# Kernel tuning notes

Hardware: AMD Instinct MI355X
Metric: run time of the kernel (lower is better)

The kernel has to match this reference:

```python
import jax, jax.numpy as jnp
import numpy as np

D_MODEL = 1024
NUM_HEADS = 16
HEAD_DIM = D_MODEL // NUM_HEADS
SCALE = HEAD_DIM ** -0.5
LN_EPS = 1e-5
Q_EPS = 1e-5


def bit_quant(W):
    # BitNet b1.58 ternary weight quantization with straight-through estimator.
    gamma = jnp.mean(jnp.abs(W))
    Wq = jnp.clip(jnp.round(W / (gamma + Q_EPS)), -1.0, 1.0) * gamma
    return W + jax.lax.stop_gradient(Wq - W)


def layer_norm(x, gamma, beta):
    mu = jnp.mean(x, axis=-1, keepdims=True)
    var = jnp.mean(jnp.square(x - mu), axis=-1, keepdims=True)
    return (x - mu) * jax.lax.rsqrt(var + LN_EPS) * gamma + beta


def setup_inputs() -> dict:
    key = jax.random.key(0)
    ks = jax.random.split(key, 8)
    B, T, T_ctx, C = 4, 1024, 2048, D_MODEL
    w_std = C ** -0.5
    return {
        "x": jax.random.normal(ks[0], (B, T, C), jnp.float32),
        "context": jax.random.normal(ks[1], (B, T_ctx, C), jnp.float32),
        "Wq": jax.random.normal(ks[2], (C, C), jnp.float32) * w_std,
        "bq": jnp.zeros((C,), jnp.float32),
        "Wk": jax.random.normal(ks[3], (C, C), jnp.float32) * w_std,
        "bk": jnp.zeros((C,), jnp.float32),
        "Wv": jax.random.normal(ks[4], (C, C), jnp.float32) * w_std,
        "bv": jnp.zeros((C,), jnp.float32),
        "Wo": jax.random.normal(ks[5], (C, C), jnp.float32) * w_std,
        "bo": jnp.zeros((C,), jnp.float32),
        "ln_gamma": jnp.ones((C,), jnp.float32),
        "ln_beta": jnp.zeros((C,), jnp.float32),
    }


def reference(x, context, Wq, bq, Wk, bk, Wv, bv, Wo, bo, ln_gamma, ln_beta):
    B, T, C = x.shape
    T_ctx = context.shape[1]
    residual = x
    xn = layer_norm(x, ln_gamma, ln_beta)
    # BitNet-quantized projections (torch Linear: y = x @ W.T + b)
    q = xn @ bit_quant(Wq).T + bq                      # [B,T,C]
    k = context @ bit_quant(Wk).T + bk                 # [B,T_ctx,C]
    v = context @ bit_quant(Wv).T + bv                 # [B,T_ctx,C]
    q = q.reshape(B, T, NUM_HEADS, HEAD_DIM)
    k = k.reshape(B, T_ctx, NUM_HEADS, HEAD_DIM)
    v = v.reshape(B, T_ctx, NUM_HEADS, HEAD_DIM)
    scores = jnp.einsum("bqhd,bkhd->bhqk", q, k) * SCALE   # [B,H,T,T_ctx]
    probs = jax.nn.softmax(scores, axis=-1)
    out = jnp.einsum("bhqk,bkhd->bqhd", probs, v).reshape(B, T, C)
    return residual + (out @ bit_quant(Wo).T + bo)
```

## Files before the change

### kernel.cpp

```cpp
#include <hip/hip_runtime.h>
#include <hip/hip_bf16.h>

typedef __attribute__((ext_vector_type(8))) short s8x;
typedef __attribute__((ext_vector_type(4))) float f4x;
typedef unsigned short u16;
typedef unsigned int u32;

#define T_ 1024
#define TC_ 2048
#define SCLOG2E 0.1803368801111243f

#define WAIT_VM(n) asm volatile("s_waitcnt vmcnt(" #n ")" ::: "memory")

__device__ __forceinline__ u16 f2bf(float f) {
    u32 u = __float_as_uint(f);
    return (u16)((u + 0x7fffu + ((u >> 16) & 1u)) >> 16);
}

#if defined(__has_builtin)
#if __has_builtin(__builtin_amdgcn_cvt_pk_bf16_f32)
#define HAVE_PK 1
#endif
#if __has_builtin(__builtin_amdgcn_permlane16_swap) && __has_builtin(__builtin_amdgcn_permlane32_swap)
#define HAVE_PLSWAP 1
#endif
#endif

__device__ __forceinline__ u32 pack2bf(float a, float b) {
#ifdef HAVE_PK
    typedef __attribute__((ext_vector_type(2))) __bf16 bf2t;
    bf2t r = __builtin_amdgcn_cvt_pk_bf16_f32(a, b);
    u32 u;
    __builtin_memcpy(&u, &r, 4);
    return u;
#else
    return (u32)f2bf(a) | ((u32)f2bf(b) << 16);
#endif
}

__device__ __forceinline__ void pswap32(u32& a, u32& b) {
#ifdef HAVE_PLSWAP
    typedef __attribute__((ext_vector_type(2))) unsigned int u2x;
    u2x r = __builtin_amdgcn_permlane32_swap(a, b, false, false);
    a = r.x; b = r.y;
#else
    asm("v_permlane32_swap_b32 %0, %1" : "+v"(a), "+v"(b));
#endif
}
__device__ __forceinline__ void pswap16(u32& a, u32& b) {
#ifdef HAVE_PLSWAP
    typedef __attribute__((ext_vector_type(2))) unsigned int u2x;
    u2x r = __builtin_amdgcn_permlane16_swap(a, b, false, false);
    a = r.x; b = r.y;
#else
    asm("v_permlane16_swap_b32 %0, %1" : "+v"(a), "+v"(b));
#endif
}

__device__ __forceinline__ void gload16(const void* g, void* l) {
    __builtin_amdgcn_global_load_lds((const __attribute__((address_space(1))) u32*)g,
                                     (__attribute__((address_space(3))) u32*)l, 16, 0, 0);
}

__global__ __launch_bounds__(256) void absmean_k(const float* __restrict__ W0, const float* __restrict__ W1,
                                                 const float* __restrict__ W2, const float* __restrict__ W3,
                                                 float* __restrict__ gsum) {
    int wi = blockIdx.y;
    const float* W = (wi == 0) ? W0 : (wi == 1) ? W1 : (wi == 2) ? W2 : W3;
    const int n4 = (1024 * 1024) / 4;
    float s = 0.f;
    int stride = gridDim.x * blockDim.x;
    for (int i = blockIdx.x * blockDim.x + threadIdx.x; i < n4; i += stride) {
        float4 v = ((const float4*)W)[i];
        s += fabsf(v.x) + fabsf(v.y) + fabsf(v.z) + fabsf(v.w);
    }
#pragma unroll
    for (int off = 32; off; off >>= 1) s += __shfl_down(s, off, 64);
    __shared__ float ps[4];
    if ((threadIdx.x & 63) == 0) ps[threadIdx.x >> 6] = s;
    __syncthreads();
    if (threadIdx.x == 0) atomicAdd(gsum + wi, ps[0] + ps[1] + ps[2] + ps[3]);
}

__global__ __launch_bounds__(256) void prep_k(
        const float* __restrict__ x, const float* __restrict__ lng, const float* __restrict__ lnb,
        u16* __restrict__ xn,
        const float* __restrict__ ctx, u16* __restrict__ ctxb,
        const float* __restrict__ W0, const float* __restrict__ W1,
        const float* __restrict__ W2, const float* __restrict__ W3,
        u16* __restrict__ D0, u16* __restrict__ D1, u16* __restrict__ D2, u16* __restrict__ D3,
        const float* __restrict__ gsum) {
    __shared__ float ps[8];
    int bx = blockIdx.x, t = threadIdx.x;
    if (bx < 4096) {
        int row = bx;
        float4 xv = ((const float4*)(x + (long)row * 1024))[t];
        float s = xv.x + xv.y + xv.z + xv.w;
        float s2 = xv.x * xv.x + xv.y * xv.y + xv.z * xv.z + xv.w * xv.w;
#pragma unroll
        for (int off = 32; off; off >>= 1) { s += __shfl_down(s, off, 64); s2 += __shfl_down(s2, off, 64); }
        if ((t & 63) == 0) { ps[t >> 6] = s; ps[4 + (t >> 6)] = s2; }
        __syncthreads();
        float S = ps[0] + ps[1] + ps[2] + ps[3];
        float S2 = ps[4] + ps[5] + ps[6] + ps[7];
        float mu = S * (1.f / 1024.f);
        float var = S2 * (1.f / 1024.f) - mu * mu;
        float rstd = rsqrtf(var + 1e-5f);
        float4 gv = ((const float4*)lng)[t];
        float4 bv = ((const float4*)lnb)[t];
        uint2 o;
        o.x = pack2bf((xv.x - mu) * rstd * gv.x + bv.x, (xv.y - mu) * rstd * gv.y + bv.y);
        o.y = pack2bf((xv.z - mu) * rstd * gv.z + bv.z, (xv.w - mu) * rstd * gv.w + bv.w);
        ((uint2*)(xn + (long)row * 1024))[t] = o;
    } else if (bx < 12288) {
        int i = (bx - 4096) * 256 + t;
        float4 v = ((const float4*)ctx)[i];
        uint2 o = {pack2bf(v.x, v.y), pack2bf(v.z, v.w)};
        ((uint2*)ctxb)[i] = o;
    } else {
        int wi = (bx - 12288) >> 10;
        const float* W = (wi == 0) ? W0 : (wi == 1) ? W1 : (wi == 2) ? W2 : W3;
        u16* D = (wi == 0) ? D0 : (wi == 1) ? D1 : (wi == 2) ? D2 : D3;
        float inv = 1.0f / (gsum[wi] * (1.0f / 1048576.0f) + 1e-5f);
        int i = ((bx - 12288) & 1023) * 256 + t;
        float4 wv = ((const float4*)W)[i];
        uint2 o;
        o.x = pack2bf(fminf(1.f, fmaxf(-1.f, rintf(wv.x * inv))),
                      fminf(1.f, fmaxf(-1.f, rintf(wv.y * inv))));
        o.y = pack2bf(fminf(1.f, fmaxf(-1.f, rintf(wv.z * inv))),
                      fminf(1.f, fmaxf(-1.f, rintf(wv.w * inv))));
        ((uint2*)D)[i] = o;
    }
}

__global__ __launch_bounds__(256) void gemm_fused(
        const u16* __restrict__ xn, const u16* __restrict__ ctxb,
        const u16* __restrict__ wtq, const u16* __restrict__ wtk, const u16* __restrict__ wtv,
        const float* __restrict__ bq, const float* __restrict__ bk, const float* __restrict__ bv,
        const float* __restrict__ gsum,
        u16* __restrict__ qb, u16* __restrict__ kb, u16* __restrict__ vtb) {
    __shared__ __align__(16) char smem[49152];
    int tid = threadIdx.x;
    int w = tid >> 6, l = tid & 63, lq = l & 15, lh = l >> 4;
    int wm = (w >> 1) * 64, wn = (w & 1) * 64;
    int bx = blockIdx.x;
    int xcd = bx & 7;
    int prob, m0, n0, gidx;
    const u16 *A, *Wt;
    const float* bias;
    float sc;
    if (bx < 256) {
        int local = bx >> 3;
        prob = 0; A = xn; Wt = wtq; bias = bq; sc = SCLOG2E; gidx = 0;
        m0 = (xcd * 4 + (local & 3)) * 128;
        n0 = (local >> 2) * 128;
    } else {
        int b = bx - 256;
        int local3 = b >> 3;
        int kv = local3 & 1;
        int idx = local3 >> 1;
        prob = 1 + kv; A = ctxb;
        Wt = kv ? wtv : wtk; bias = kv ? bv : bk; sc = 1.0f; gidx = 1 + kv;
        m0 = (xcd * 8 + (idx & 7)) * 128;
        n0 = (idx >> 3) * 128;
    }
    int sp = tid >> 3, ss = tid & 7;
    int st = ss ^ (sp & 7);
    int r0 = sp * 2 + (st >> 2), c0 = st & 3;
    const u16* Ag0 = A + (long)(m0 + r0) * 1024 + c0 * 8;
    const u16* Ag1 = Ag0 + 64 * 1024;
    const u16* Bg0 = Wt + (long)(n0 + r0) * 1024 + c0 * 8;
    const u16* Bg1 = Bg0 + 64 * 1024;
    int aoff[4], boff[4];
#pragma unroll
    for (int i = 0; i < 4; i++) {
        int ar = wm + i * 16 + lq, ap = ar >> 1;
        aoff[i] = ap * 128 + (((((ar & 1) << 2) | lh) ^ (ap & 7)) * 16);
        int br = wn + i * 16 + lq, bp = br >> 1;
        boff[i] = bp * 128 + (((((br & 1) << 2) | lh) ^ (bp & 7)) * 16);
    }
    f4x acc[4][4] = {};
#define STAGE_G(kt, buf)                                                   \
    {                                                                      \
        char* Ad = smem + (buf) * 16384;                                   \
        char* Bd = Ad + 8192;                                              \
        gload16(Ag0 + (kt) * 32, Ad + tid * 16);                           \
        gload16(Ag1 + (kt) * 32, Ad + 4096 + tid * 16);                    \
        gload16(Bg0 + (kt) * 32, Bd + tid * 16);                           \
        gload16(Bg1 + (kt) * 32, Bd + 4096 + tid * 16);                    \
    }
    STAGE_G(0, 0);
    STAGE_G(1, 1);
#pragma unroll
    for (int kt = 0; kt < 32; kt++) {
        if (kt < 31) { WAIT_VM(4); } else { WAIT_VM(0); }
        __builtin_amdgcn_s_barrier();
        if (kt + 2 < 32) STAGE_G(kt + 2, (kt + 2) % 3);
        const char* Ac = smem + (kt % 3) * 16384;
        const char* Bc = Ac + 8192;
        s8x af[4], bfr[4];
#pragma unroll
        for (int i = 0; i < 4; i++) {
            af[i] = *(const s8x*)(Ac + aoff[i]);
            bfr[i] = *(const s8x*)(Bc + boff[i]);
        }
#pragma unroll
        for (int i = 0; i < 4; i++)
#pragma unroll
            for (int j = 0; j < 4; j++)
                acc[i][j] = __builtin_amdgcn_mfma_f32_16x16x32_bf16(af[i], bfr[j], acc[i][j], 0, 0, 0);
    }
    float gamma = gsum[gidx] * (1.0f / 1048576.0f) * sc;
    if (prob < 2) {
        u16* outq = (prob == 0) ? qb : kb;
        int tshift = (prob == 0) ? 10 : 11;
        int tmask = (1 << tshift) - 1;
#pragma unroll
        for (int i = 0; i < 4; i++) {
            int gr = m0 + wm + i * 16 + lh * 4;
#pragma unroll
            for (int j = 0; j < 4; j++) {
                int gc = n0 + wn + j * 16 + lq;
                float bb = bias[gc] * sc;
                int h = gc >> 6, d = gc & 63;
#pragma unroll
                for (int r = 0; r < 4; r++) {
                    int row = gr + r;
                    int bidx = row >> tshift, tt = row & tmask;
                    outq[((((long)(bidx * 16 + h)) << tshift) + tt) * 64 + d] = f2bf(acc[i][j][r] * gamma + bb);
                }
            }
        }
    } else {
        __syncthreads();
        char* Ct = smem;
#pragma unroll
        for (int i = 0; i < 4; i++) {
            int tt = wm + i * 16 + lh * 4;
#pragma unroll
            for (int j = 0; j < 4; j++) {
                int c = wn + j * 16 + lq;
                float bb = bias[n0 + c];
                uint2 pk;
                pk.x = pack2bf(acc[i][j][0] * gamma + bb, acc[i][j][1] * gamma + bb);
                pk.y = pack2bf(acc[i][j][2] * gamma + bb, acc[i][j][3] * gamma + bb);
                int slot = (tt >> 3) ^ (c & 15);
                *(uint2*)(Ct + c * 256 + slot * 16 + (tt & 7) * 2) = pk;
            }
        }
        __syncthreads();
        int bb2 = m0 >> 11, t0 = m0 & 2047;
#pragma unroll
        for (int it = 0; it < 8; it++) {
            int e = it * 256 + tid;
            int c = e >> 4, ch = e & 15;
            int slot = ch ^ (c & 15);
            s8x v = *(const s8x*)(Ct + c * 256 + slot * 16);
            int gcg = n0 + c;
            int h = gcg >> 6, d = gcg & 63;
            *(s8x*)(vtb + ((long)((bb2 * 16 + h) * 64 + d)) * TC_ + t0 + ch * 8) = v;
        }
    }
}

__global__ __launch_bounds__(256) void gemm_o(const u16* __restrict__ A, const u16* __restrict__ Wt,
                                              const float* __restrict__ bias, const float* __restrict__ gsum,
                                              const float* __restrict__ residual, float* __restrict__ outr) {
    __shared__ __align__(16) char smem[36864];
    int tid = threadIdx.x;
    int w = tid >> 6, l = tid & 63, lq = l & 15, lh = l >> 4;
    int wm = (w >> 1) * 64, wn = (w & 1) * 32;
    int bx = blockIdx.x;
    int xcd = bx & 7, local = bx >> 3;
    int m0 = (xcd * 4 + (local & 3)) * 128;
    int n0 = (local >> 2) * 64;
    int sp = tid >> 3, ss = tid & 7;
    int st = ss ^ (sp & 7);
    int r0 = sp * 2 + (st >> 2), c0 = st & 3;
    const u16* Ag0 = A + (long)(m0 + r0) * 1024 + c0 * 8;
    const u16* Ag1 = Ag0 + 64 * 1024;
    const u16* Bg0 = Wt + (long)(n0 + r0) * 1024 + c0 * 8;
    int aoff[4], boff[2];
#pragma unroll
    for (int i = 0; i < 4; i++) {
        int ar = wm + i * 16 + lq, ap = ar >> 1;
        aoff[i] = ap * 128 + (((((ar & 1) << 2) | lh) ^ (ap & 7)) * 16);
    }
#pragma unroll
    for (int j = 0; j < 2; j++) {
        int br = wn + j * 16 + lq, bp = br >> 1;
        boff[j] = bp * 128 + (((((br & 1) << 2) | lh) ^ (bp & 7)) * 16);
    }
    f4x acc[4][2] = {};
#define STAGE_O(kt, buf)                                                   \
    {                                                                      \
        char* Ad = smem + (buf) * 12288;                                   \
        char* Bd = Ad + 8192;                                              \
        gload16(Ag0 + (kt) * 32, Ad + tid * 16);                           \
        gload16(Ag1 + (kt) * 32, Ad + 4096 + tid * 16);                    \
        gload16(Bg0 + (kt) * 32, Bd + tid * 16);                           \
    }
    STAGE_O(0, 0);
    STAGE_O(1, 1);
#pragma unroll
    for (int kt = 0; kt < 32; kt++) {
        if (kt < 31) { WAIT_VM(3); } else { WAIT_VM(0); }
        __builtin_amdgcn_s_barrier();
        if (kt + 2 < 32) STAGE_O(kt + 2, (kt + 2) % 3);
        const char* Ac = smem + (kt % 3) * 12288;
        const char* Bc = Ac + 8192;
        s8x af[4], bfr[2];
#pragma unroll
        for (int i = 0; i < 4; i++) af[i] = *(const s8x*)(Ac + aoff[i]);
#pragma unroll
        for (int j = 0; j < 2; j++) bfr[j] = *(const s8x*)(Bc + boff[j]);
#pragma unroll
        for (int i = 0; i < 4; i++)
#pragma unroll
            for (int j = 0; j < 2; j++)
                acc[i][j] = __builtin_amdgcn_mfma_f32_16x16x32_bf16(af[i], bfr[j], acc[i][j], 0, 0, 0);
    }
    float gamma = gsum[3] * (1.0f / 1048576.0f);
#pragma unroll
    for (int i = 0; i < 4; i++) {
        int gr = m0 + wm + i * 16 + lh * 4;
#pragma unroll
        for (int j = 0; j < 2; j++) {
            int gc = n0 + wn + j * 16 + lq;
            float bb = bias[gc];
#pragma unroll
            for (int r = 0; r < 4; r++) {
                long idx = (long)(gr + r) * 1024 + gc;
                outr[idx] = residual[idx] + acc[i][j][r] * gamma + bb;
            }
        }
    }
}

__global__ __launch_bounds__(256) void attn_k(const u16* __restrict__ qh, const u16* __restrict__ kh,
                                              const u16* __restrict__ vth, u16* __restrict__ attn) {
    __shared__ __align__(16) char smem[32768];
    int tid = threadIdx.x, w = tid >> 6, l = tid & 63, lq = l & 15, lh = l >> 4;
    int bh = blockIdx.x, q0 = blockIdx.y * 128;
    const u16* qp = qh + ((long)bh * T_ + q0) * 64;
    const u16* kp = kh + (long)bh * TC_ * 64;
    const u16* vp = vth + (long)bh * 64 * TC_;
#pragma unroll
    for (int i = 0; i < 4; i++) {
        int cid = i * 256 + tid;
        int r = cid >> 3, c = (cid & 7) ^ (r & 7);
        gload16(qp + r * 64 + c * 8, smem + cid * 16);
    }
    __syncthreads();
    s8x qf[2][2];
#pragma unroll
    for (int qb = 0; qb < 2; qb++)
#pragma unroll
        for (int dh = 0; dh < 2; dh++) {
            int qrow = w * 32 + qb * 16 + lq;
            int ch = (dh * 4 + lh) ^ (qrow & 7);
            qf[qb][dh] = *(const s8x*)(smem + qrow * 128 + ch * 16);
        }
    __syncthreads();
#define STAGE_KV(kt, buf)                                                          \
    {                                                                              \
        char* Kb = smem + (buf) * 16384;                                           \
        char* Vb = Kb + 8192;                                                      \
        _Pragma("unroll") for (int i = 0; i < 2; i++) {                            \
            int cid = i * 256 + tid;                                               \
            int r = cid >> 3, c = (cid & 7) ^ (r & 7);                             \
            gload16(kp + ((kt) * 64 + r) * 64 + c * 8, Kb + cid * 16);             \
            gload16(vp + (long)r * TC_ + (kt) * 64 + c * 8, Vb + cid * 16);        \
        }                                                                          \
    }
    STAGE_KV(0, 0);
    f4x oacc[2][4] = {};
    f4x lrun[2] = {};
    const s8x ones = {16256, 16256, 16256, 16256, 16256, 16256, 16256, 16256};
    for (int kt = 0; kt < TC_ / 64; kt++) {
        __syncthreads();
        if (kt + 1 < TC_ / 64) STAGE_KV(kt + 1, (kt + 1) & 1);
        char* Ksb = smem + (kt & 1) * 16384;
        char* Vsb = Ksb + 8192;
        f4x z[2][4];
        __builtin_amdgcn_s_setprio(1);
#pragma unroll
        for (int ni = 0; ni < 4; ni++) {
            int kr = ni * 16 + lq;
            s8x a0 = *(const s8x*)(Ksb + kr * 128 + ((lh) ^ (kr & 7)) * 16);
            s8x a1 = *(const s8x*)(Ksb + kr * 128 + ((4 + lh) ^ (kr & 7)) * 16);
#pragma unroll
            for (int qb = 0; qb < 2; qb++) {
                f4x zz = {0.f, 0.f, 0.f, 0.f};
                zz = __builtin_amdgcn_mfma_f32_16x16x32_bf16(a0, qf[qb][0], zz, 0, 0, 0);
                zz = __builtin_amdgcn_mfma_f32_16x16x32_bf16(a1, qf[qb][1], zz, 0, 0, 0);
                z[qb][ni] = zz;
            }
        }
        __builtin_amdgcn_s_setprio(0);
        s8x vf[4][2];
#pragma unroll
        for (int nd = 0; nd < 4; nd++) {
            int vr = nd * 16 + lq;
            vf[nd][0] = *(const s8x*)(Vsb + vr * 128 + ((lh) ^ (vr & 7)) * 16);
            vf[nd][1] = *(const s8x*)(Vsb + vr * 128 + ((4 + lh) ^ (vr & 7)) * 16);
        }
#pragma unroll
        for (int qb = 0; qb < 2; qb++) {
            u32 Wp[4][2];
#pragma unroll
            for (int ni = 0; ni < 4; ni++) {
                Wp[ni][0] = pack2bf(__builtin_amdgcn_exp2f(z[qb][ni][0]), __builtin_amdgcn_exp2f(z[qb][ni][1]));
                Wp[ni][1] = pack2bf(__builtin_amdgcn_exp2f(z[qb][ni][2]), __builtin_amdgcn_exp2f(z[qb][ni][3]));
            }
            u32 a0w = Wp[0][0], a1w = Wp[1][0]; pswap32(a0w, a1w); pswap16(a0w, a1w);
            u32 b0w = Wp[0][1], b1w = Wp[1][1]; pswap32(b0w, b1w); pswap16(b0w, b1w);
            u32 c0w = Wp[2][0], c1w = Wp[3][0]; pswap32(c0w, c1w); pswap16(c0w, c1w);
            u32 d0w = Wp[2][1], d1w = Wp[3][1]; pswap32(d0w, d1w); pswap16(d0w, d1w);
            u32 pw0[4] = {a0w, b0w, a1w, b1w};
            u32 pw1[4] = {c0w, d0w, c1w, d1w};
            s8x pf0, pf1;
            __builtin_memcpy(&pf0, pw0, 16);
            __builtin_memcpy(&pf1, pw1, 16);
            __builtin_amdgcn_s_setprio(1);
            f4x rs = {0.f, 0.f, 0.f, 0.f};
            rs = __builtin_amdgcn_mfma_f32_16x16x32_bf16(pf0, ones, rs, 0, 0, 0);
            rs = __builtin_amdgcn_mfma_f32_16x16x32_bf16(pf1, ones, rs, 0, 0, 0);
#pragma unroll
            for (int r = 0; r < 4; r++) lrun[qb][r] += rs[r];
#pragma unroll
            for (int nd = 0; nd < 4; nd++) {
                oacc[qb][nd] = __builtin_amdgcn_mfma_f32_16x16x32_bf16(pf0, vf[nd][0], oacc[qb][nd], 0, 0, 0);
                oacc[qb][nd] = __builtin_amdgcn_mfma_f32_16x16x32_bf16(pf1, vf[nd][1], oacc[qb][nd], 0, 0, 0);
            }
            __builtin_amdgcn_s_setprio(0);
        }
    }
    int b = bh >> 4, h = bh & 15;
#pragma unroll
    for (int qb = 0; qb < 2; qb++)
#pragma unroll
        for (int r = 0; r < 4; r++) {
            int q = q0 + w * 32 + qb * 16 + lh * 4 + r;
            float rcp = 1.f / lrun[qb][r];
#pragma unroll
            for (int nd = 0; nd < 4; nd++)
                attn[((long)(b * T_ + q)) * 1024 + h * 64 + nd * 16 + lq] = f2bf(oacc[qb][nd][r] * rcp);
        }
}

extern "C" void kernel_launch(void* const* d_in, const int* in_sizes, int n_in,
                              void* d_out, int out_size, void* d_ws, size_t ws_size,
                              hipStream_t stream) {
    const float* x   = (const float*)d_in[0];
    const float* ctx = (const float*)d_in[1];
    const float* Wq  = (const float*)d_in[2];
    const float* bq  = (const float*)d_in[3];
    const float* Wk  = (const float*)d_in[4];
    const float* bk  = (const float*)d_in[5];
    const float* Wv  = (const float*)d_in[6];
    const float* bv  = (const float*)d_in[7];
    const float* Wo  = (const float*)d_in[8];
    const float* bo  = (const float*)d_in[9];
    const float* lng = (const float*)d_in[10];
    const float* lnb = (const float*)d_in[11];
    float* out = (float*)d_out;

    char* ws = (char*)d_ws;
    float* gsum = (float*)ws;
    size_t off = 256;
    u16* wtq  = (u16*)(ws + off); off += (size_t)1024 * 1024 * 2;
    u16* wtk  = (u16*)(ws + off); off += (size_t)1024 * 1024 * 2;
    u16* wtv  = (u16*)(ws + off); off += (size_t)1024 * 1024 * 2;
    u16* wto  = (u16*)(ws + off); off += (size_t)1024 * 1024 * 2;
    u16* ctxb = (u16*)(ws + off); off += (size_t)8192 * 1024 * 2;
    u16* xn   = (u16*)(ws + off); off += (size_t)4096 * 1024 * 2;
    u16* qb_  = (u16*)(ws + off); off += (size_t)4096 * 1024 * 2;
    u16* kb   = (u16*)(ws + off); off += (size_t)8192 * 1024 * 2;
    u16* vtb  = (u16*)(ws + off); off += (size_t)8192 * 1024 * 2;
    u16* attnb = xn;

    hipMemsetAsync(gsum, 0, 16, stream);
    absmean_k<<<dim3(128, 4), 256, 0, stream>>>(Wq, Wk, Wv, Wo, gsum);
    prep_k<<<16384, 256, 0, stream>>>(x, lng, lnb, xn, ctx, ctxb,
                                      Wq, Wk, Wv, Wo, wtq, wtk, wtv, wto, gsum);
    gemm_fused<<<1280, 256, 0, stream>>>(xn, ctxb, wtq, wtk, wtv, bq, bk, bv, gsum, qb_, kb, vtb);
    attn_k<<<dim3(64, 8), 256, 0, stream>>>(qb_, kb, vtb, attnb);
    gemm_o<<<512, 256, 0, stream>>>(attnb, wto, bo, gsum, x, out);
}
```

Baseline: 254.2 us.

## Software-pipeline attention loop with 4-stage KV ring and overlapped QK/softmax

Restructures the attention kernel's KV loop into a 4-buffer shared-memory ring (64KB LDS), prefetching three tiles ahead with explicit vmcnt waits and raw barriers instead of __syncthreads. QK^T scores for the next tile are computed while exp2 and PV of the current tile proceed, so MFMA work overlaps transcendental and permute work. Row-sum accumulation now goes straight into the MFMA accumulator, and global/LDS pointers are precomputed and advanced incrementally. The larger LDS footprint and doubled score registers may limit occupancy, which launch_bounds(256,2) tries to keep at two blocks.

```diff
diff --git a/kernel.cpp b/kernel.cpp
--- a/kernel.cpp
+++ b/kernel.cpp
@@ -337,14 +337,12 @@
     }
 }
 
-__global__ __launch_bounds__(256) void attn_k(const u16* __restrict__ qh, const u16* __restrict__ kh,
-                                              const u16* __restrict__ vth, u16* __restrict__ attn) {
-    __shared__ __align__(16) char smem[32768];
+__global__ __launch_bounds__(256, 2) void attn_k(const u16* __restrict__ qh, const u16* __restrict__ kh,
+                                                 const u16* __restrict__ vth, u16* __restrict__ attn) {
+    __shared__ __align__(16) char smem[65536];
     int tid = threadIdx.x, w = tid >> 6, l = tid & 63, lq = l & 15, lh = l >> 4;
     int bh = blockIdx.x, q0 = blockIdx.y * 128;
     const u16* qp = qh + ((long)bh * T_ + q0) * 64;
-    const u16* kp = kh + (long)bh * TC_ * 64;
-    const u16* vp = vth + (long)bh * 64 * TC_;
 #pragma unroll
     for (int i = 0; i < 4; i++) {
         int cid = i * 256 + tid;
@@ -362,79 +360,136 @@
             qf[qb][dh] = *(const s8x*)(smem + qrow * 128 + ch * 16);
         }
     __syncthreads();
-#define STAGE_KV(kt, buf)                                                          \
-    {                                                                              \
-        char* Kb = smem + (buf) * 16384;                                           \
-        char* Vb = Kb + 8192;                                                      \
-        _Pragma("unroll") for (int i = 0; i < 2; i++) {                            \
-            int cid = i * 256 + tid;                                               \
-            int r = cid >> 3, c = (cid & 7) ^ (r & 7);                             \
-            gload16(kp + ((kt) * 64 + r) * 64 + c * 8, Kb + cid * 16);             \
-            gload16(vp + (long)r * TC_ + (kt) * 64 + c * 8, Vb + cid * 16);        \
-        }                                                                          \
-    }
-    STAGE_KV(0, 0);
+    int sr = tid >> 3, sc = (tid & 7) ^ ((tid >> 3) & 7);
+    const u16* kgA = kh + (long)bh * TC_ * 64 + sr * 64 + sc * 8;
+    const u16* kgB = kgA + 2048;
+    const u16* vgA = vth + (long)bh * 64 * TC_ + (long)sr * TC_ + sc * 8;
+    const u16* vgB = vgA + 32 * TC_;
+    const char* pA = smem + lq * 128 + ((lh ^ (lq & 7)) * 16);
+    const char* pB = smem + lq * 128 + (((4 + lh) ^ (lq & 7)) * 16);
+#define STAGE4(buf)                                              \
+    {                                                            \
+        char* Kb = smem + (buf) * 16384;                         \
+        gload16(kgA, Kb + tid * 16);                             \
+        gload16(kgB, Kb + 4096 + tid * 16);                      \
+        gload16(vgA, Kb + 8192 + tid * 16);                      \
+        gload16(vgB, Kb + 12288 + tid * 16);                     \
+        kgA += 4096; kgB += 4096; vgA += 64; vgB += 64;          \
+    }
+#define SM1(ZA, qb, PF0, PF1)                                                                              \
+    s8x PF0, PF1;                                                                                          \
+    {                                                                                                      \
+        u32 w00 = pack2bf(__builtin_amdgcn_exp2f(ZA[qb][0][0]), __builtin_amdgcn_exp2f(ZA[qb][0][1]));     \
+        u32 w01 = pack2bf(__builtin_amdgcn_exp2f(ZA[qb][0][2]), __builtin_amdgcn_exp2f(ZA[qb][0][3]));     \
+        u32 w10 = pack2bf(__builtin_amdgcn_exp2f(ZA[qb][1][0]), __builtin_amdgcn_exp2f(ZA[qb][1][1]));     \
+        u32 w11 = pack2bf(__builtin_amdgcn_exp2f(ZA[qb][1][2]), __builtin_amdgcn_exp2f(ZA[qb][1][3]));     \
+        u32 w20 = pack2bf(__builtin_amdgcn_exp2f(ZA[qb][2][0]), __builtin_amdgcn_exp2f(ZA[qb][2][1]));     \
+        u32 w21 = pack2bf(__builtin_amdgcn_exp2f(ZA[qb][2][2]), __builtin_amdgcn_exp2f(ZA[qb][2][3]));     \
+        u32 w30 = pack2bf(__builtin_amdgcn_exp2f(ZA[qb][3][0]), __builtin_amdgcn_exp2f(ZA[qb][3][1]));     \
+        u32 w31 = pack2bf(__builtin_amdgcn_exp2f(ZA[qb][3][2]), __builtin_amdgcn_exp2f(ZA[qb][3][3]));     \
+        u32 a0w = w00, a1w = w10; pswap32(a0w, a1w); pswap16(a0w, a1w);                                    \
+        u32 b0w = w01, b1w = w11; pswap32(b0w, b1w); pswap16(b0w, b1w);                                    \
+        u32 c0w = w20, c1w = w30; pswap32(c0w, c1w); pswap16(c0w, c1w);                                    \
+        u32 d0w = w21, d1w = w31; pswap32(d0w, d1w); pswap16(d0w, d1w);                                    \
+        u32 pw0[4] = {a0w, b0w, a1w, b1w};                                                                 \
+        u32 pw1[4] = {c0w, d0w, c1w, d1w};                                                                 \
+        __builtin_memcpy(&PF0, pw0, 16);                                                                   \
+        __builtin_memcpy(&PF1, pw1, 16);                                                                   \
+    }
+#define SUBITER(JB, KB, SB, ZC, ZN, WN, DOSTAGE)                                                           \
+    {                                                                                                      \
+        WAIT_VM(WN);                                                                                       \
+        __builtin_amdgcn_s_barrier();                                                                      \
+        if (DOSTAGE) STAGE4(SB);                                                                           \
+        s8x a0_[4], a1_[4], v0_[4], v1_[4];                                                                \
+        _Pragma("unroll") for (int ni = 0; ni < 4; ni++) {                                                 \
+            a0_[ni] = *(const s8x*)(pA + (KB) * 16384 + ni * 2048);                                        \
+            a1_[ni] = *(const s8x*)(pB + (KB) * 16384 + ni * 2048);                                        \
+        }                                                                                                  \
+        _Pragma("unroll") for (int nd = 0; nd < 4; nd++) {                                                 \
+            v0_[nd] = *(const s8x*)(pA + (JB) * 16384 + 8192 + nd * 2048);                                 \
+            v1_[nd] = *(const s8x*)(pB + (JB) * 16384 + 8192 + nd * 2048);                                 \
+        }                                                                                                  \
+        SM1(ZC, 0, pfa0, pfa1)                                                                             \
+        __builtin_amdgcn_s_setprio(1);                                                                     \
+        _Pragma("unroll") for (int ni = 0; ni < 4; ni++) {                                                 \
+            _Pragma("unroll") for (int qb = 0; qb < 2; qb++) {                                             \
+                f4x zz = {0.f, 0.f, 0.f, 0.f};                                                             \
+                zz = __builtin_amdgcn_mfma_f32_16x16x32_bf16(a0_[ni], qf[qb][0], zz, 0, 0, 0);             \
+                zz = __builtin_amdgcn_mfma_f32_16x16x32_bf16(a1_[ni], qf[qb][1], zz, 0, 0, 0);             \
+                ZN[qb][ni] = zz;                                                                           \
+            }                                                                                              \
+        }                                                                                                  \
+        __builtin_amdgcn_s_setprio(0);                                                                     \
+        SM1(ZC, 1, pfb0, pfb1)                                                                             \
+        __builtin_amdgcn_s_setprio(1);                                                                     \
+        lrun[0] = __builtin_amdgcn_mfma_f32_16x16x32_bf16(pfa0, ones, lrun[0], 0, 0, 0);                   \
+        lrun[0] = __builtin_amdgcn_mfma_f32_16x16x32_bf16(pfa1, ones, lrun[0], 0, 0, 0);                   \
+        lrun[1] = __builtin_amdgcn_mfma_f32_16x16x32_bf16(pfb0, ones, lrun[1], 0, 0, 0);                   \
+        lrun[1] = __builtin_amdgcn_mfma_f32_16x16x32_bf16(pfb1, ones, lrun[1], 0, 0, 0);                   \
+        _Pragma("unroll") for (int nd = 0; nd < 4; nd++) {                                                 \
+            oacc[0][nd] = __builtin_amdgcn_mfma_f32_16x16x32_bf16(pfa0, v0_[nd], oacc[0][nd], 0, 0, 0);    \
+            oacc[0][nd] = __builtin_amdgcn_mfma_f32_16x16x32_bf16(pfa1, v1_[nd], oacc[0][nd], 0, 0, 0);    \
+            oacc[1][nd] = __builtin_amdgcn_mfma_f32_16x16x32_bf16(pfb0, v0_[nd], oacc[1][nd], 0, 0, 0);    \
+            oacc[1][nd] = __builtin_amdgcn_mfma_f32_16x16x32_bf16(pfb1, v1_[nd], oacc[1][nd], 0, 0, 0);    \
+        }                                                                                                  \
+        __builtin_amdgcn_s_setprio(0);                                                                     \
+    }
+    const s8x ones = {16256, 16256, 16256, 16256, 16256, 16256, 16256, 16256};
+    f4x z0[2][4], z1[2][4];
     f4x oacc[2][4] = {};
     f4x lrun[2] = {};
-    const s8x ones = {16256, 16256, 16256, 16256, 16256, 16256, 16256, 16256};
-    for (int kt = 0; kt < TC_ / 64; kt++) {
-        __syncthreads();
-        if (kt + 1 < TC_ / 64) STAGE_KV(kt + 1, (kt + 1) & 1);
-        char* Ksb = smem + (kt & 1) * 16384;
-        char* Vsb = Ksb + 8192;
-        f4x z[2][4];
-        __builtin_amdgcn_s_setprio(1);
+    STAGE4(0); STAGE4(1); STAGE4(2);
+    WAIT_VM(8);
+    __builtin_amdgcn_s_barrier();
+    {
+        s8x a0_[4], a1_[4];
 #pragma unroll
         for (int ni = 0; ni < 4; ni++) {
-            int kr = ni * 16 + lq;
-            s8x a0 = *(const s8x*)(Ksb + kr * 128 + ((lh) ^ (kr & 7)) * 16);
-            s8x a1 = *(const s8x*)(Ksb + kr * 128 + ((4 + lh) ^ (kr & 7)) * 16);
+            a0_[ni] = *(const s8x*)(pA + ni * 2048);
+            a1_[ni] = *(const s8x*)(pB + ni * 2048);
+        }
+#pragma unroll
+        for (int ni = 0; ni < 4; ni++)
 #pragma unroll
             for (int qb = 0; qb < 2; qb++) {
                 f4x zz = {0.f, 0.f, 0.f, 0.f};
-                zz = __builtin_amdgcn_mfma_f32_16x16x32_bf16(a0, qf[qb][0], zz, 0, 0, 0);
-                zz = __builtin_amdgcn_mfma_f32_16x16x32_bf16(a1, qf[qb][1], zz, 0, 0, 0);
-                z[qb][ni] = zz;
+                zz = __builtin_amdgcn_mfma_f32_16x16x32_bf16(a0_[ni], qf[qb][0], zz, 0, 0, 0);
+                zz = __builtin_amdgcn_mfma_f32_16x16x32_bf16(a1_[ni], qf[qb][1], zz, 0, 0, 0);
+                z0[qb][ni] = zz;
             }
+    }
+    for (int t = 0; t < 7; t++) {
+        SUBITER(0, 1, 3, z0, z1, 4, true)
+        SUBITER(1, 2, 0, z1, z0, 4, true)
+        SUBITER(2, 3, 1, z0, z1, 4, true)
+        SUBITER(3, 0, 2, z1, z0, 4, true)
+    }
+    SUBITER(0, 1, 3, z0, z1, 4, true)
+    SUBITER(1, 2, 0, z1, z0, 4, false)
+    SUBITER(2, 3, 1, z0, z1, 0, false)
+    {
+        s8x v0_[4], v1_[4];
+#pragma unroll
+        for (int nd = 0; nd < 4; nd++) {
+            v0_[nd] = *(const s8x*)(pA + 3 * 16384 + 8192 + nd * 2048);
+            v1_[nd] = *(const s8x*)(pB + 3 * 16384 + 8192 + nd * 2048);
+        }
+        SM1(z1, 0, pfa0, pfa1)
+        SM1(z1, 1, pfb0, pfb1)
+        __builtin_amdgcn_s_setprio(1);
+        lrun[0] = __builtin_amdgcn_mfma_f32_16x16x32_bf16(pfa0, ones, lrun[0], 0, 0, 0);
+        lrun[0] = __builtin_amdgcn_mfma_f32_16x16x32_bf16(pfa1, ones, lrun[0], 0, 0, 0);
+        lrun[1] = __builtin_amdgcn_mfma_f32_16x16x32_bf16(pfb0, ones, lrun[1], 0, 0, 0);
+        lrun[1] = __builtin_amdgcn_mfma_f32_16x16x32_bf16(pfb1, ones, lrun[1], 0, 0, 0);
+#pragma unroll
+        for (int nd = 0; nd < 4; nd++) {
+            oacc[0][nd] = __builtin_amdgcn_mfma_f32_16x16x32_bf16(pfa0, v0_[nd], oacc[0][nd], 0, 0, 0);
+            oacc[0][nd] = __builtin_amdgcn_mfma_f32_16x16x32_bf16(pfa1, v1_[nd], oacc[0][nd], 0, 0, 0);
+            oacc[1][nd] = __builtin_amdgcn_mfma_f32_16x16x32_bf16(pfb0, v0_[nd], oacc[1][nd], 0, 0, 0);
+            oacc[1][nd] = __builtin_amdgcn_mfma_f32_16x16x32_bf16(pfb1, v1_[nd], oacc[1][nd], 0, 0, 0);
         }
         __builtin_amdgcn_s_setprio(0);
-        s8x vf[4][2];
-#pragma unroll
-        for (int nd = 0; nd < 4; nd++) {
-            int vr = nd * 16 + lq;
-            vf[nd][0] = *(const s8x*)(Vsb + vr * 128 + ((lh) ^ (vr & 7)) * 16);
-            vf[nd][1] = *(const s8x*)(Vsb + vr * 128 + ((4 + lh) ^ (vr & 7)) * 16);
-        }
-#pragma unroll
-        for (int qb = 0; qb < 2; qb++) {
-            u32 Wp[4][2];
-#pragma unroll
-            for (int ni = 0; ni < 4; ni++) {
-                Wp[ni][0] = pack2bf(__builtin_amdgcn_exp2f(z[qb][ni][0]), __builtin_amdgcn_exp2f(z[qb][ni][1]));
-                Wp[ni][1] = pack2bf(__builtin_amdgcn_exp2f(z[qb][ni][2]), __builtin_amdgcn_exp2f(z[qb][ni][3]));
-            }
-            u32 a0w = Wp[0][0], a1w = Wp[1][0]; pswap32(a0w, a1w); pswap16(a0w, a1w);
-            u32 b0w = Wp[0][1], b1w = Wp[1][1]; pswap32(b0w, b1w); pswap16(b0w, b1w);
-            u32 c0w = Wp[2][0], c1w = Wp[3][0]; pswap32(c0w, c1w); pswap16(c0w, c1w);
-            u32 d0w = Wp[2][1], d1w = Wp[3][1]; pswap32(d0w, d1w); pswap16(d0w, d1w);
-            u32 pw0[4] = {a0w, b0w, a1w, b1w};
-            u32 pw1[4] = {c0w, d0w, c1w, d1w};
-            s8x pf0, pf1;
-            __builtin_memcpy(&pf0, pw0, 16);
-            __builtin_memcpy(&pf1, pw1, 16);
-            __builtin_amdgcn_s_setprio(1);
-            f4x rs = {0.f, 0.f, 0.f, 0.f};
-            rs = __builtin_amdgcn_mfma_f32_16x16x32_bf16(pf0, ones, rs, 0, 0, 0);
-            rs = __builtin_amdgcn_mfma_f32_16x16x32_bf16(pf1, ones, rs, 0, 0, 0);
-#pragma unroll
-            for (int r = 0; r < 4; r++) lrun[qb][r] += rs[r];
-#pragma unroll
-            for (int nd = 0; nd < 4; nd++) {
-                oacc[qb][nd] = __builtin_amdgcn_mfma_f32_16x16x32_bf16(pf0, vf[nd][0], oacc[qb][nd], 0, 0, 0);
-                oacc[qb][nd] = __builtin_amdgcn_mfma_f32_16x16x32_bf16(pf1, vf[nd][1], oacc[qb][nd], 0, 0, 0);
-            }
-            __builtin_amdgcn_s_setprio(0);
-        }
     }
     int b = bh >> 4, h = bh & 15;
 #pragma unroll
```

Result: faster. 243.4 us (-4.3%).
